# Performance work log

Measured on AMD Instinct MI355X. Metric: run time of the kernel, lower is better.

## Reference

```python
import jax, jax.numpy as jnp
import numpy as np

THRESHOLD = 23.0
LN_EPS = 1e-5


def setup_inputs() -> dict:
    key = jax.random.key(0)
    ks = jax.random.split(key, 8)
    B, N, D, F = 8, 4096, 256, 1024
    xavier_fc = (6.0 / (D + D)) ** 0.5
    xavier_1 = (6.0 / (D + F)) ** 0.5
    xavier_2 = (6.0 / (F + D)) ** 0.5
    return {
        "discriminative_query": jax.random.normal(ks[0], (B, N, D), dtype=jnp.float32),
        "indiscriminative_query": jax.random.normal(ks[1], (B, N, D), dtype=jnp.float32),
        "W_fc": jax.random.uniform(ks[2], (D, D), jnp.float32, -xavier_fc, xavier_fc),
        "b_fc": jnp.zeros((D,), jnp.float32),
        "W1": jax.random.uniform(ks[3], (F, D), jnp.float32, -xavier_1, xavier_1),
        "b1": jnp.zeros((F,), jnp.float32),
        "W2": jax.random.uniform(ks[4], (D, F), jnp.float32, -xavier_2, xavier_2),
        "b2": jnp.zeros((D,), jnp.float32),
        "ln_g": jnp.ones((D,), jnp.float32),
        "ln_b": jnp.zeros((D,), jnp.float32),
    }


def _mean_agg(path, X):
    # path: [B, r, c] incidence; X: [B, c, d] -> mean over incident nodes
    out = jnp.einsum("brc,bcd->brd", path, X)
    deg = jnp.sum(path, axis=2, keepdims=True)  # [B, r, 1]
    norm = jnp.where(deg > 0, 1.0 / deg, 0.0)
    return norm * out


def reference(discriminative_query, indiscriminative_query,
              W_fc, b_fc, W1, b1, W2, b2, ln_g, ln_b):
    f1 = indiscriminative_query  # [B, Nv, D]
    f2 = discriminative_query    # [B, Ne, D]
    # torch.cdist (p=2): euclidean distance via squared-norm expansion
    sq = (jnp.sum(f1 * f1, axis=-1)[:, :, None]
          + jnp.sum(f2 * f2, axis=-1)[:, None, :]
          - 2.0 * jnp.einsum("bnd,bmd->bnm", f1, f2))
    dist = jnp.sqrt(jnp.maximum(sq, 0.0))
    hg = (dist < THRESHOLD).astype(f1.dtype)  # [B, Nv, Ne]

    # HyPConv
    X = jnp.einsum("bnd,ed->bne", indiscriminative_query, W_fc) + b_fc
    Ht = jnp.swapaxes(hg, 1, 2)               # [B, Ne, Nv]
    E = _mean_agg(Ht, X) + discriminative_query  # [B, Ne, D]
    v = _mean_agg(hg, E)                         # [B, Nv, D]

    enhanced = v + indiscriminative_query

    # FFN (dropout=0 / eval mode)
    h = jax.nn.relu(jnp.einsum("bnd,fd->bnf", enhanced, W1) + b1)
    src2 = jnp.einsum("bnf,df->bnd", h, W2) + b2
    q = enhanced + src2

    # LayerNorm
    mu = jnp.mean(q, axis=-1, keepdims=True)
    var = jnp.mean((q - mu) ** 2, axis=-1, keepdims=True)
    return (q - mu) * jax.lax.rsqrt(var + LN_EPS) * ln_g + ln_b
```

## Files before the change

### kernel.cpp

```cpp
#include <hip/hip_runtime.h>
#include <stdint.h>


typedef unsigned short u16;
typedef __attribute__((ext_vector_type(8))) short bf16x8;
typedef __attribute__((ext_vector_type(4))) float f32x4;

#define GLDS(g, l) __builtin_amdgcn_global_load_lds((const __attribute__((address_space(1))) void*)(g), (__attribute__((address_space(3))) void*)(l), 16, 0, 0)

__device__ __forceinline__ float4 ld4(const float* p){ return *reinterpret_cast<const float4*>(p); }
__device__ __forceinline__ u16 f2bf(float f){
    union{float f;unsigned u;}x{f};
    unsigned r=(x.u+0x7FFFu+((x.u>>16)&1u))>>16; return (u16)r;
}
__device__ __forceinline__ float bf2f(u16 s){
    union{unsigned u;float f;}x{(unsigned)s<<16}; return x.f;
}
__device__ __forceinline__ unsigned pk2(unsigned v, int i){
    return (((v>>i)&1u)*0x3F80u) | (((v>>(i+1))&1u)*0x3F800000u);
}

template<int EPI, bool SPLIT, bool ABITS, bool BBITS>
__global__ __launch_bounds__(256)
void mg(const u16* __restrict__ A, const u16* __restrict__ A2,
        const u16* __restrict__ Bt, const u16* __restrict__ B2,
        void* __restrict__ C, void* __restrict__ C2,
        int K, int lda, int ldb, int ldc,
        long long sA, long long sB, long long sC, long long sC2,
        const float* __restrict__ bias,
        const float* __restrict__ v1, long long sv1,
        const float* __restrict__ v2, long long sv2,
        const void* __restrict__ resid, long long sR)
{
    __shared__ u16 As[4096], Bs[4096];
    __shared__ u16 As2[SPLIT ? 4096 : 8], Bs2[SPLIT ? 4096 : 8];
    const int t = threadIdx.x, lane = t & 63, wv = t >> 6;
    const int i0 = blockIdx.x*128, j0 = blockIdx.y*128, z = blockIdx.z;
    const int wr = (wv>>1)*64, wc = (wv&1)*64;

    const u16* Az  = A  + (size_t)z*sA;
    const u16* Bz  = Bt + (size_t)z*sB;
    const u16* A2z = SPLIT ? A2 + (size_t)z*sA : nullptr;
    const u16* B2z = SPLIT ? B2 + (size_t)z*sB : nullptr;

    const int glr = lane >> 2;
    const int gsc = (lane & 3) ^ ((glr >> 1) & 3);
    const int frow = lane & 15;
    const int fcho = ((lane >> 4) ^ ((frow >> 1) & 3)) * 8;

    f32x4 zero4 = {0.f,0.f,0.f,0.f};
    f32x4 acc[4][4];
    #pragma unroll
    for (int m=0;m<4;++m)
        #pragma unroll
        for (int n=0;n<4;++n) acc[m][n] = zero4;

    for (int k0 = 0; k0 < K; k0 += 32) {
        if constexpr (ABITS) {
            const int row = t & 127, half = t >> 7, sw = (row>>1)&3;
            unsigned v = Az[(size_t)(i0+row)*lda + (k0>>4) + half];
            u16* base = As + row*32;
            uint4 w0, w1;
            w0.x=pk2(v,0);  w0.y=pk2(v,2);  w0.z=pk2(v,4);  w0.w=pk2(v,6);
            w1.x=pk2(v,8);  w1.y=pk2(v,10); w1.z=pk2(v,12); w1.w=pk2(v,14);
            *(uint4*)(base + ((2*half  )^sw)*8) = w0;
            *(uint4*)(base + ((2*half+1)^sw)*8) = w1;
        } else {
            #pragma unroll
            for (int q=0;q<2;++q) {
                const int lr = wv*32 + q*16 + glr;
                GLDS(Az + (size_t)(i0+lr)*lda + k0 + gsc*8, As + (wv*32 + q*16)*32);
            }
        }
        if constexpr (BBITS) {
            const int row = t & 127, half = t >> 7, sw = (row>>1)&3;
            unsigned v = Bz[(size_t)(j0+row)*ldb + (k0>>4) + half];
            u16* base = Bs + row*32;
            uint4 w0, w1;
            w0.x=pk2(v,0);  w0.y=pk2(v,2);  w0.z=pk2(v,4);  w0.w=pk2(v,6);
            w1.x=pk2(v,8);  w1.y=pk2(v,10); w1.z=pk2(v,12); w1.w=pk2(v,14);
            *(uint4*)(base + ((2*half  )^sw)*8) = w0;
            *(uint4*)(base + ((2*half+1)^sw)*8) = w1;
        } else {
            #pragma unroll
            for (int q=0;q<2;++q) {
                const int lr = wv*32 + q*16 + glr;
                GLDS(Bz + (size_t)(j0+lr)*ldb + k0 + gsc*8, Bs + (wv*32 + q*16)*32);
            }
        }
        if constexpr (SPLIT) {
            #pragma unroll
            for (int q=0;q<2;++q) {
                const int lr = wv*32 + q*16 + glr;
                GLDS(A2z + (size_t)(i0+lr)*lda + k0 + gsc*8, As2 + (wv*32 + q*16)*32);
                GLDS(B2z + (size_t)(j0+lr)*ldb + k0 + gsc*8, Bs2 + (wv*32 + q*16)*32);
            }
        }
        __syncthreads();

        bf16x8 fa[4], fb[4];
        #pragma unroll
        for (int m=0;m<4;++m) fa[m] = *(const bf16x8*)&As[(wr + m*16 + frow)*32 + fcho];
        #pragma unroll
        for (int n=0;n<4;++n) fb[n] = *(const bf16x8*)&Bs[(wc + n*16 + frow)*32 + fcho];
        if constexpr (SPLIT) {
            bf16x8 fa2[4], fb2[4];
            #pragma unroll
            for (int m=0;m<4;++m) fa2[m] = *(const bf16x8*)&As2[(wr + m*16 + frow)*32 + fcho];
            #pragma unroll
            for (int n=0;n<4;++n) fb2[n] = *(const bf16x8*)&Bs2[(wc + n*16 + frow)*32 + fcho];
            #pragma unroll
            for (int m=0;m<4;++m)
                #pragma unroll
                for (int n=0;n<4;++n) {
                    acc[m][n] = __builtin_amdgcn_mfma_f32_16x16x32_bf16(fa[m],  fb[n],  acc[m][n], 0,0,0);
                    acc[m][n] = __builtin_amdgcn_mfma_f32_16x16x32_bf16(fa[m],  fb2[n], acc[m][n], 0,0,0);
                    acc[m][n] = __builtin_amdgcn_mfma_f32_16x16x32_bf16(fa2[m], fb[n],  acc[m][n], 0,0,0);
                }
        } else {
            #pragma unroll
            for (int m=0;m<4;++m)
                #pragma unroll
                for (int n=0;n<4;++n)
                    acc[m][n] = __builtin_amdgcn_mfma_f32_16x16x32_bf16(fa[m], fb[n], acc[m][n], 0,0,0);
        }
        __syncthreads();
    }

    const int cl = lane & 15, rg = lane >> 4;
    if constexpr (EPI == 1) {
        u16* hgb  = (u16*)C  + (size_t)z*sC;
        u16* hgtb = (u16*)C2 + (size_t)z*sC2;
        const float* v1z = v1 + (size_t)z*sv1;
        const float* v2z = v2 + (size_t)z*sv2;
        #pragma unroll
        for (int m=0;m<4;++m) {
            #pragma unroll
            for (int n=0;n<4;++n) {
                const int rb = i0 + wr + m*16;
                const int cb = j0 + wc + n*16;
                const float n2c = v2z[cb + cl];
                unsigned long long b0,b1,b2,b3;
                { float s = v1z[rb+rg*4+0] + n2c - 2.f*acc[m][n][0]; b0 = __ballot(s < 529.f); }
                { float s = v1z[rb+rg*4+1] + n2c - 2.f*acc[m][n][1]; b1 = __ballot(s < 529.f); }
                { float s = v1z[rb+rg*4+2] + n2c - 2.f*acc[m][n][2]; b2 = __ballot(s < 529.f); }
                { float s = v1z[rb+rg*4+3] + n2c - 2.f*acc[m][n][3]; b3 = __ballot(s < 529.f); }
                unsigned long long bsel = (cl&2) ? ((cl&1)? b3 : b2) : ((cl&1)? b1 : b0);
                if (cl < 4)
                    hgb[(size_t)(rb + rg*4 + cl)*ldc + (cb>>4)] = (u16)((bsel >> (rg*16)) & 0xFFFFull);
                if (rg == 0) {
                    unsigned tb = 0;
                    #pragma unroll
                    for (int k=0;k<16;++k) {
                        unsigned long long bb = (k&2) ? ((k&1)? b3:b2) : ((k&1)? b1:b0);
                        tb |= (unsigned)((bb >> ((k>>2)*16 + cl)) & 1ull) << k;
                    }
                    hgtb[(size_t)(cb + cl)*ldc + (rb>>4)] = (u16)tb;
                }
            }
        }
    } else {
        float* Cf  = (float*)C  + (size_t)z*sC;
        u16*   Cb  = (u16*)C    + (size_t)z*sC;
        u16*   C2b = (u16*)C2   + (size_t)z*sC2;
        const float* Rf = (const float*)resid + (size_t)z*sR;
        const u16*   Rb = (const u16*)resid   + (size_t)z*sR;
        const float* v1z = v1 ? v1 + (size_t)z*sv1 : nullptr;
        const float* v2z = v2 ? v2 + (size_t)z*sv2 : nullptr;
        #pragma unroll
        for (int m=0;m<4;++m) {
            #pragma unroll
            for (int n=0;n<4;++n) {
                const int cc = j0 + wc + n*16 + cl;
                #pragma unroll
                for (int j=0;j<4;++j) {
                    const int r = i0 + wr + m*16 + rg*4 + j;
                    const float v = acc[m][n][j];
                    if constexpr (EPI == 0) {
                        Cb[(size_t)r*ldc + cc] = f2bf(v + bias[r]);
                    } else if constexpr (EPI == 2) {
                        float d = v2z[cc]; float nm = d > 0.f ? 1.f/d : 0.f;
                        Cb[(size_t)r*ldc + cc] = f2bf(v*nm + bf2f(Rb[(size_t)r*ldc + cc]));
                    } else if constexpr (EPI == 3) {
                        float d = v1z[r]; float nm = d > 0.f ? 1.f/d : 0.f;
                        float o = v*nm + Rf[(size_t)r*ldc + cc];
                        Cf [(size_t)r*ldc + cc] = o;
                        C2b[(size_t)r*ldc + cc] = f2bf(o);
                    } else if constexpr (EPI == 4) {
                        float o = v + bias[cc];
                        Cb[(size_t)r*ldc + cc] = f2bf(o > 0.f ? o : 0.f);
                    } else {
                        Cf[(size_t)r*ldc + cc] = v + bias[cc] + Rf[(size_t)r*ldc + cc];
                    }
                }
            }
        }
    }
}

__global__ __launch_bounds__(256)
void prep_k(const float* __restrict__ ind, const float* __restrict__ disc,
            u16* __restrict__ ih, u16* __restrict__ dh,
            float* __restrict__ n1, float* __restrict__ n2, int rows)
{
    int wid = threadIdx.x >> 6, lane = threadIdx.x & 63;
    int r = blockIdx.x*4 + wid;
    const float* src; u16 *hi; float* dst; int rr;
    if (r < rows) { src = ind;  hi = ih; dst = n1; rr = r; }
    else          { src = disc; hi = dh; dst = n2; rr = r - rows; }
    size_t off = (size_t)rr*256 + lane*4;
    float4 v = ld4(src + off);
    ushort4 h;
    h.x = f2bf(v.x); h.y = f2bf(v.y); h.z = f2bf(v.z); h.w = f2bf(v.w);
    *(ushort4*)(hi+off) = h;
    float s = v.x*v.x + v.y*v.y + v.z*v.z + v.w*v.w;
    #pragma unroll
    for (int o=32;o;o>>=1) s += __shfl_down(s, o);
    if (lane == 0) dst[rr] = s;
}

__global__ __launch_bounds__(256)
void cvtw_k(const float* __restrict__ wfc, const float* __restrict__ w1,
            const float* __restrict__ w2, u16* __restrict__ owfc,
            u16* __restrict__ ow1, u16* __restrict__ ow2)
{
    int i = blockIdx.x*256 + threadIdx.x;
    if (i < 65536)  owfc[i] = f2bf(wfc[i]);
    if (i < 262144) { ow1[i] = f2bf(w1[i]); ow2[i] = f2bf(w2[i]); }
}

__global__ __launch_bounds__(256)
void tr_k(const float* __restrict__ src, u16* __restrict__ dst)
{
    __shared__ float tl[64][65];
    const int b = blockIdx.z, n0 = blockIdx.x*64, d0 = blockIdx.y*64;
    const float* s = src + (size_t)b*1048576;
    u16* o = dst + (size_t)b*1048576;
    const int tx = threadIdx.x & 15, ty = threadIdx.x >> 4;
    #pragma unroll
    for (int it=0; it<4; ++it) {
        int r = ty + it*16;
        float4 v = ld4(s + (size_t)(n0+r)*256 + d0 + tx*4);
        tl[r][tx*4+0]=v.x; tl[r][tx*4+1]=v.y; tl[r][tx*4+2]=v.z; tl[r][tx*4+3]=v.w;
    }
    __syncthreads();
    #pragma unroll
    for (int it=0; it<4; ++it) {
        int d = ty + it*16;
        ushort4 w;
        w.x = f2bf(tl[tx*4+0][d]); w.y = f2bf(tl[tx*4+1][d]);
        w.z = f2bf(tl[tx*4+2][d]); w.w = f2bf(tl[tx*4+3][d]);
        *(ushort4*)(o + (size_t)(d0+d)*4096 + n0 + tx*4) = w;
    }
}

__global__ __launch_bounds__(256)
void popc_k(const u16* __restrict__ bits, float* __restrict__ deg)
{
    int wv = threadIdx.x >> 6, lane = threadIdx.x & 63;
    size_t row = (size_t)blockIdx.x*4 + wv;
    const unsigned* p = (const unsigned*)(bits + row*256);
    int s = __popc(p[lane]) + __popc(p[lane+64]);
    #pragma unroll
    for (int o=32;o;o>>=1) s += __shfl_down(s, o);
    if (lane == 0) deg[row] = (float)s;
}

__global__ __launch_bounds__(256)
void ln_k(const float* __restrict__ q, const float* __restrict__ g,
          const float* __restrict__ bta, float* __restrict__ out)
{
    size_t row = blockIdx.x;
    int t = threadIdx.x;
    float x = q[row*256 + t];
    float s1 = x, s2 = x*x;
    int lane = t & 63, wid = t >> 6;
    #pragma unroll
    for (int o=32;o;o>>=1) { s1 += __shfl_down(s1,o); s2 += __shfl_down(s2,o); }
    __shared__ float a1[4], a2[4];
    if (lane == 0) { a1[wid]=s1; a2[wid]=s2; }
    __syncthreads();
    s1 = a1[0]+a1[1]+a1[2]+a1[3];
    s2 = a2[0]+a2[1]+a2[2]+a2[3];
    float mu  = s1 * (1.f/256.f);
    float var = s2 * (1.f/256.f) - mu*mu;
    float r = rsqrtf(var + 1e-5f);
    out[row*256 + t] = (x - mu) * r * g[t] + bta[t];
}

extern "C" void kernel_launch(void* const* d_in, const int* in_sizes, int n_in,
                              void* d_out, int out_size, void* d_ws, size_t ws_size,
                              hipStream_t stream)
{
    const float* disc = (const float*)d_in[0];
    const float* ind  = (const float*)d_in[1];
    const float* W_fc = (const float*)d_in[2];
    const float* b_fc = (const float*)d_in[3];
    const float* W1   = (const float*)d_in[4];
    const float* b1   = (const float*)d_in[5];
    const float* W2   = (const float*)d_in[6];
    const float* b2   = (const float*)d_in[7];
    const float* ln_g = (const float*)d_in[8];
    const float* ln_b = (const float*)d_in[9];
    float* out = (float*)d_out;

    char* ws = (char*)d_ws;
    u16* hgb   = (u16*)(ws + 0);
    u16* hgtb  = (u16*)(ws + 16777216);
    u16* ETb   = (u16*)(ws + 33554432);
    u16* ih    = (u16*)(ws + 50331648);
    u16* dh    = (u16*)(ws + 83886080);
    u16* discT = (u16*)(ws + 117440512);
    u16* XTb   = (u16*)(ws + 134217728);
    float* enhF= (float*)(ws + 150994944);
    u16* enhB  = (u16*)(ws + 184549376);
    u16* wfcb  = (u16*)(ws + 201326592);
    u16* w1b   = (u16*)(ws + 201457664);
    u16* w2b   = (u16*)(ws + 201981952);
    float* n1  = (float*)(ws + 202506240);
    float* n2  = (float*)(ws + 202637312);
    float* dN  = (float*)(ws + 202768384);
    float* dE  = (float*)(ws + 202899456);
    u16* hB    = (u16*)(ws + 83886080);
    float* qF  = (float*)(ws + 50331648);

    const int BN = 32768;
    const long long S = 1048576;

    prep_k<<<16384, 256, 0, stream>>>(ind, disc, ih, dh, n1, n2, BN);
    cvtw_k<<<1024, 256, 0, stream>>>(W_fc, W1, W2, wfcb, w1b, w2b);
    tr_k<<<dim3(64,4,8), 256, 0, stream>>>(disc, discT);

    mg<1,false,false,false><<<dim3(32,32,8), 256, 0, stream>>>(
        ih, nullptr, dh, nullptr, hgb, hgtb, 256, 256, 256, 256,
        S, S, S, S, nullptr, n1, 4096, n2, 4096, nullptr, 0);

    popc_k<<<8192, 256, 0, stream>>>(hgb,  dN);
    popc_k<<<8192, 256, 0, stream>>>(hgtb, dE);

    mg<0,false,false,false><<<dim3(2,32,8), 256, 0, stream>>>(
        wfcb, nullptr, ih, nullptr, XTb, nullptr, 256, 256, 256, 4096,
        0, S, S, 0, b_fc, nullptr, 0, nullptr, 0, nullptr, 0);

    mg<2,false,false,true><<<dim3(2,32,8), 256, 0, stream>>>(
        XTb, nullptr, hgtb, nullptr, ETb, nullptr, 4096, 4096, 256, 4096,
        S, S, S, 0, nullptr, nullptr, 0, dE, 4096, discT, S);

    mg<3,false,true,false><<<dim3(32,2,8), 256, 0, stream>>>(
        hgb, nullptr, ETb, nullptr, enhF, enhB, 4096, 256, 4096, 256,
        S, S, S, S, nullptr, dN, 4096, nullptr, 0, ind, S);

    mg<4,false,false,false><<<dim3(256,8,1), 256, 0, stream>>>(
        enhB, nullptr, w1b, nullptr, hB, nullptr, 256, 256, 256, 1024,
        0, 0, 0, 0, b1, nullptr, 0, nullptr, 0, nullptr, 0);

    mg<5,false,false,false><<<dim3(256,2,1), 256, 0, stream>>>(
        hB, nullptr, w2b, nullptr, qF, nullptr, 1024, 1024, 1024, 256,
        0, 0, 0, 0, b2, nullptr, 0, nullptr, 0, enhF, 0);

    ln_k<<<BN, 256, 0, stream>>>(qF, ln_g, ln_b, out);
}
```

Before: 633.7 us.

## Add dedicated 128x256 aggregation GEMM kernel for hypergraph mean-aggregation steps

Introduces a new 512-thread kernel `ag` with 128x256 output tiles for the two aggregation GEMMs that read the bit-packed incidence matrix. The bits are expanded to bf16 while loading into LDS, and the degree normalisation plus residual are applied in the epilogue. Wider tiles mean each unpacked incidence tile is reused across more output columns and fewer blocks are launched. The old EPI 2/3 paths are removed from the generic kernel. Grids shrink, for example 32x1x8 = 256 blocks for the second GEMM, which may underfill the GPU's compute units.

```diff
diff --git a/kernel.cpp b/kernel.cpp
--- a/kernel.cpp
+++ b/kernel.cpp
@@ -162,11 +162,7 @@
     } else {
         float* Cf  = (float*)C  + (size_t)z*sC;
         u16*   Cb  = (u16*)C    + (size_t)z*sC;
-        u16*   C2b = (u16*)C2   + (size_t)z*sC2;
         const float* Rf = (const float*)resid + (size_t)z*sR;
-        const u16*   Rb = (const u16*)resid   + (size_t)z*sR;
-        const float* v1z = v1 ? v1 + (size_t)z*sv1 : nullptr;
-        const float* v2z = v2 ? v2 + (size_t)z*sv2 : nullptr;
         #pragma unroll
         for (int m=0;m<4;++m) {
             #pragma unroll
@@ -178,20 +174,124 @@
                     const float v = acc[m][n][j];
                     if constexpr (EPI == 0) {
                         Cb[(size_t)r*ldc + cc] = f2bf(v + bias[r]);
-                    } else if constexpr (EPI == 2) {
-                        float d = v2z[cc]; float nm = d > 0.f ? 1.f/d : 0.f;
-                        Cb[(size_t)r*ldc + cc] = f2bf(v*nm + bf2f(Rb[(size_t)r*ldc + cc]));
-                    } else if constexpr (EPI == 3) {
-                        float d = v1z[r]; float nm = d > 0.f ? 1.f/d : 0.f;
-                        float o = v*nm + Rf[(size_t)r*ldc + cc];
-                        Cf [(size_t)r*ldc + cc] = o;
-                        C2b[(size_t)r*ldc + cc] = f2bf(o);
                     } else if constexpr (EPI == 4) {
                         float o = v + bias[cc];
                         Cb[(size_t)r*ldc + cc] = f2bf(o > 0.f ? o : 0.f);
                     } else {
                         Cf[(size_t)r*ldc + cc] = v + bias[cc] + Rf[(size_t)r*ldc + cc];
                     }
+                }
+            }
+        }
+    }
+}
+
+template<int EPI>
+__global__ __launch_bounds__(512)
+void ag(const u16* __restrict__ A, const u16* __restrict__ Bt,
+        void* __restrict__ C, void* __restrict__ C2,
+        int K, int lda, int ldb, int ldc,
+        long long sA, long long sB, long long sC, long long sC2,
+        const float* __restrict__ deg, long long sdeg,
+        const void* __restrict__ resid, long long sR)
+{
+    __shared__ u16 As[4096];
+    __shared__ u16 Bs[8192];
+    const int t = threadIdx.x, lane = t & 63, wv = t >> 6;
+    const int i0 = blockIdx.x*128, j0 = blockIdx.y*256, z = blockIdx.z;
+    const int wr = (wv>>2)*64, wc = (wv&3)*64;
+
+    const u16* Az = A  + (size_t)z*sA;
+    const u16* Bz = Bt + (size_t)z*sB;
+
+    const int glr = lane >> 2;
+    const int gsc = (lane & 3) ^ ((glr >> 1) & 3);
+    const int frow = lane & 15;
+    const int fcho = ((lane >> 4) ^ ((frow >> 1) & 3)) * 8;
+
+    f32x4 zero4 = {0.f,0.f,0.f,0.f};
+    f32x4 acc[4][4];
+    #pragma unroll
+    for (int m=0;m<4;++m)
+        #pragma unroll
+        for (int n=0;n<4;++n) acc[m][n] = zero4;
+
+    for (int k0 = 0; k0 < K; k0 += 32) {
+        if constexpr (EPI == 3) {
+            const int r = t & 127, q = t >> 7, sw = (r>>1)&3;
+            unsigned v32 = *(const unsigned*)(Az + (size_t)(i0+r)*lda + (k0>>4));
+            unsigned b = (v32 >> (q*8)) & 0xFFu;
+            uint4 w;
+            w.x = pk2(b,0); w.y = pk2(b,2); w.z = pk2(b,4); w.w = pk2(b,6);
+            *(uint4*)(As + r*32 + (q ^ sw)*8) = w;
+        } else {
+            GLDS(Az + (size_t)(i0 + wv*16 + glr)*lda + k0 + gsc*8, As + (wv*16)*32);
+        }
+        if constexpr (EPI == 2) {
+            const int r = t & 255, h = t >> 8, sw = (r>>1)&3;
+            unsigned v = Bz[(size_t)(j0+r)*ldb + (k0>>4) + h];
+            u16* base = Bs + r*32;
+            uint4 w0, w1;
+            w0.x=pk2(v,0);  w0.y=pk2(v,2);  w0.z=pk2(v,4);  w0.w=pk2(v,6);
+            w1.x=pk2(v,8);  w1.y=pk2(v,10); w1.z=pk2(v,12); w1.w=pk2(v,14);
+            *(uint4*)(base + ((2*h  )^sw)*8) = w0;
+            *(uint4*)(base + ((2*h+1)^sw)*8) = w1;
+        } else {
+            #pragma unroll
+            for (int q=0;q<2;++q) {
+                const int rb = q*128 + wv*16;
+                GLDS(Bz + (size_t)(j0 + rb + glr)*ldb + k0 + gsc*8, Bs + rb*32);
+            }
+        }
+        __syncthreads();
+
+        bf16x8 fa[4], fb[4];
+        #pragma unroll
+        for (int m=0;m<4;++m) fa[m] = *(const bf16x8*)&As[(wr + m*16 + frow)*32 + fcho];
+        #pragma unroll
+        for (int n=0;n<4;++n) fb[n] = *(const bf16x8*)&Bs[(wc + n*16 + frow)*32 + fcho];
+        #pragma unroll
+        for (int m=0;m<4;++m)
+            #pragma unroll
+            for (int n=0;n<4;++n)
+                acc[m][n] = __builtin_amdgcn_mfma_f32_16x16x32_bf16(fa[m], fb[n], acc[m][n], 0,0,0);
+        __syncthreads();
+    }
+
+    const int cl = lane & 15, rg = lane >> 4;
+    const float* degz = deg + (size_t)z*sdeg;
+    if constexpr (EPI == 2) {
+        u16* Cb = (u16*)C + (size_t)z*sC;
+        const u16* Rb = (const u16*)resid + (size_t)z*sR;
+        #pragma unroll
+        for (int m=0;m<4;++m) {
+            #pragma unroll
+            for (int n=0;n<4;++n) {
+                const int cc = j0 + wc + n*16 + cl;
+                float d = degz[cc]; float nm = d > 0.f ? 1.f/d : 0.f;
+                #pragma unroll
+                for (int j=0;j<4;++j) {
+                    const int r = i0 + wr + m*16 + rg*4 + j;
+                    Cb[(size_t)r*ldc + cc] = f2bf(acc[m][n][j]*nm + bf2f(Rb[(size_t)r*ldc + cc]));
+                }
+            }
+        }
+    } else {
+        float* Cf  = (float*)C  + (size_t)z*sC;
+        u16*   C2b = (u16*)C2   + (size_t)z*sC2;
+        const float* Rf = (const float*)resid + (size_t)z*sR;
+        #pragma unroll
+        for (int m=0;m<4;++m) {
+            #pragma unroll
+            for (int n=0;n<4;++n) {
+                const int cc = j0 + wc + n*16 + cl;
+                #pragma unroll
+                for (int j=0;j<4;++j) {
+                    const int r = i0 + wr + m*16 + rg*4 + j;
+                    float d = degz[r]; float nm = d > 0.f ? 1.f/d : 0.f;
+                    float o = acc[m][n][j]*nm + Rf[(size_t)r*ldc + cc];
+                    Cf [(size_t)r*ldc + cc] = o;
+                    C2b[(size_t)r*ldc + cc] = f2bf(o);
                 }
             }
         }
@@ -342,13 +442,13 @@
         wfcb, nullptr, ih, nullptr, XTb, nullptr, 256, 256, 256, 4096,
         0, S, S, 0, b_fc, nullptr, 0, nullptr, 0, nullptr, 0);
 
-    mg<2,false,false,true><<<dim3(2,32,8), 256, 0, stream>>>(
-        XTb, nullptr, hgtb, nullptr, ETb, nullptr, 4096, 4096, 256, 4096,
-        S, S, S, 0, nullptr, nullptr, 0, dE, 4096, discT, S);
-
-    mg<3,false,true,false><<<dim3(32,2,8), 256, 0, stream>>>(
-        hgb, nullptr, ETb, nullptr, enhF, enhB, 4096, 256, 4096, 256,
-        S, S, S, S, nullptr, dN, 4096, nullptr, 0, ind, S);
+    ag<2><<<dim3(2,16,8), 512, 0, stream>>>(
+        XTb, hgtb, ETb, nullptr, 4096, 4096, 256, 4096,
+        S, S, S, 0, dE, 4096, discT, S);
+
+    ag<3><<<dim3(32,1,8), 512, 0, stream>>>(
+        hgb, ETb, enhF, enhB, 4096, 256, 4096, 256,
+        S, S, S, S, dN, 4096, ind, S);
 
     mg<4,false,false,false><<<dim3(256,8,1), 256, 0, stream>>>(
         enhB, nullptr, w1b, nullptr, hB, nullptr, 256, 256, 256, 1024,
```

Measured after the change: 677.7 us. 6.9% more time.
